# Performance work log

Measured on AMD Instinct MI355X. Metric: run time of the kernel, lower is better.

The kernel has to match this reference:

```python
import jax, jax.numpy as jnp
import numpy as np

EPS = 1e-8


def setup_inputs() -> dict:
    key = jax.random.key(0)
    kx, kw, kb = jax.random.split(key, 3)
    B, S, K, N = 64, 4096, 256, 256
    x = jax.random.normal(kx, (B, S, K), dtype=jnp.float32)
    # Kaiming-uniform-ish init for weight (out_features, in_features)
    bound_w = np.sqrt(6.0 / K) / np.sqrt(1.0 + 5.0)  # kaiming_uniform with a=sqrt(5)
    weight = jax.random.uniform(kw, (N, K), dtype=jnp.float32, minval=-bound_w, maxval=bound_w)
    bound_b = 1.0 / np.sqrt(K)
    bias = jax.random.uniform(kb, (N,), dtype=jnp.float32, minval=-bound_b, maxval=bound_b)
    return {"x": x, "weight": weight, "bias": bias}


def reference(x, weight, bias):
    """LNS inference path of LNSLinear.

    log_out[m, n] = logsumexp_k(log(|x[m,k]|+eps) + log(|w[n,k]|+eps))
    out = sign(sign(x) @ sign(w).T) * exp(log_out) + bias
    Computed stably as log(exp(lx - mx) @ exp(lw - mw).T) + mx + mw.
    """
    orig_shape = x.shape
    K = weight.shape[1]
    xf = x.reshape(-1, K)                                  # [M, K]
    log_x = jnp.log(jnp.abs(xf) + EPS)                     # [M, K]
    x_sign = jnp.sign(xf)                                  # [M, K]
    log_w = jnp.log(jnp.abs(weight) + EPS)                 # [N, K]
    w_sign = jnp.sign(weight)                              # [N, K]

    mx = jnp.max(log_x, axis=-1, keepdims=True)            # [M, 1]
    mw = jnp.max(log_w, axis=-1, keepdims=True)            # [N, 1]
    # logsumexp over k without materializing [M, N, K]
    acc = jnp.einsum('mk,nk->mn', jnp.exp(log_x - mx), jnp.exp(log_w - mw))
    log_out = jnp.log(acc) + mx + mw.T                     # [M, N]

    out_sign = jnp.sign(jnp.einsum('mk,nk->mn', x_sign, w_sign))
    out = out_sign * jnp.exp(log_out) + bias
    return out.reshape(orig_shape[:-1] + (weight.shape[0],))
```

## Files before the change

kernel.cpp:

```cpp
#include <hip/hip_runtime.h>
#include <hip/hip_bf16.h>
#include <stdint.h>


#define K_DIM 256
#define N_DIM 256
#define BM 128
#define BN 128
#define BK 32
#define LDK 40

typedef float f32x4 __attribute__((ext_vector_type(4)));
typedef __bf16 bf16x4 __attribute__((ext_vector_type(4)));
typedef __bf16 bf16x8 __attribute__((ext_vector_type(8)));
typedef unsigned short u16x4v __attribute__((ext_vector_type(4)));
typedef unsigned short u16x8v __attribute__((ext_vector_type(8)));

__device__ __forceinline__ void store_abs_sgn(float4 v, unsigned short* pa, unsigned short* ps) {
    bf16x4 h;
    h[0] = (__bf16)__builtin_fabsf(v.x);
    h[1] = (__bf16)__builtin_fabsf(v.y);
    h[2] = (__bf16)__builtin_fabsf(v.z);
    h[3] = (__bf16)__builtin_fabsf(v.w);
    unsigned int u0 = __float_as_uint(v.x), u1 = __float_as_uint(v.y);
    unsigned int u2 = __float_as_uint(v.z), u3 = __float_as_uint(v.w);
    u16x4v s;
    s[0] = (unsigned short)(0x3F80u | ((u0 >> 16) & 0x8000u));
    s[1] = (unsigned short)(0x3F80u | ((u1 >> 16) & 0x8000u));
    s[2] = (unsigned short)(0x3F80u | ((u2 >> 16) & 0x8000u));
    s[3] = (unsigned short)(0x3F80u | ((u3 >> 16) & 0x8000u));
    *(u16x4v*)pa = __builtin_bit_cast(u16x4v, h);
    *(u16x4v*)ps = s;
}

__global__ __launch_bounds__(256, 2)
void lns_gemm_kernel(const float* __restrict__ X, const float* __restrict__ W,
                     const float* __restrict__ bias, float* __restrict__ out, int M) {
    __shared__ unsigned short sAabs[BM * LDK];
    __shared__ unsigned short sAsgn[BM * LDK];
    __shared__ unsigned short sBabs[BN * LDK];
    __shared__ unsigned short sBsgn[BN * LDK];

    const int tid  = threadIdx.x;
    const int lane = tid & 63;
    const int wave = tid >> 6;
    const int quad = lane >> 4;
    const int l16  = lane & 15;
    const int mb   = blockIdx.y;
    const int nb   = blockIdx.x;
    const int wm   = (wave >> 1) * 64;
    const int wn   = (wave & 1) * 64;

    const float* Ax = X + (size_t)(mb * BM) * K_DIM;
    const float* Bw = W + (size_t)(nb * BN) * K_DIM;

    f32x4 accP[4][4];
    f32x4 accS[4][4];
#pragma unroll
    for (int i = 0; i < 4; ++i)
#pragma unroll
        for (int j = 0; j < 4; ++j) {
            accP[i][j] = (f32x4)(0.0f);
            accS[i][j] = (f32x4)(0.0f);
        }

    for (int k0 = 0; k0 < K_DIM; k0 += BK) {
        __syncthreads();
#pragma unroll
        for (int i = 0; i < 4; ++i) {
            int f   = i * 256 + tid;
            int row = f >> 3;
            int kc  = (f & 7) << 2;
            float4 va = *(const float4*)(Ax + (size_t)row * K_DIM + k0 + kc);
            store_abs_sgn(va, &sAabs[row * LDK + kc], &sAsgn[row * LDK + kc]);
            float4 vb = *(const float4*)(Bw + (size_t)row * K_DIM + k0 + kc);
            store_abs_sgn(vb, &sBabs[row * LDK + kc], &sBsgn[row * LDK + kc]);
        }
        __syncthreads();

        bf16x8 aab[4], asg[4], bab[4], bsg[4];
#pragma unroll
        for (int mi = 0; mi < 4; ++mi) {
            int off = (wm + mi * 16 + l16) * LDK + quad * 8;
            aab[mi] = __builtin_bit_cast(bf16x8, *(const u16x8v*)(sAabs + off));
            asg[mi] = __builtin_bit_cast(bf16x8, *(const u16x8v*)(sAsgn + off));
        }
#pragma unroll
        for (int ni = 0; ni < 4; ++ni) {
            int off = (wn + ni * 16 + l16) * LDK + quad * 8;
            bab[ni] = __builtin_bit_cast(bf16x8, *(const u16x8v*)(sBabs + off));
            bsg[ni] = __builtin_bit_cast(bf16x8, *(const u16x8v*)(sBsgn + off));
        }
#pragma unroll
        for (int mi = 0; mi < 4; ++mi)
#pragma unroll
            for (int ni = 0; ni < 4; ++ni) {
                accP[mi][ni] = __builtin_amdgcn_mfma_f32_16x16x32_bf16(
                    aab[mi], bab[ni], accP[mi][ni], 0, 0, 0);
                accS[mi][ni] = __builtin_amdgcn_mfma_f32_16x16x32_bf16(
                    asg[mi], bsg[ni], accS[mi][ni], 0, 0, 0);
            }
    }

#pragma unroll
    for (int ni = 0; ni < 4; ++ni) {
        int n   = nb * BN + wn + ni * 16 + l16;
        float b = bias[n];
#pragma unroll
        for (int mi = 0; mi < 4; ++mi) {
            int mbase = mb * BM + wm + mi * 16 + quad * 4;
#pragma unroll
            for (int r = 0; r < 4; ++r) {
                float p = accP[mi][ni][r];
                float s = accS[mi][ni][r];
                float v = (s > 0.0f) ? p : ((s < 0.0f) ? -p : 0.0f);
                out[(size_t)(mbase + r) * N_DIM + n] = v + b;
            }
        }
    }
}

extern "C" void kernel_launch(void* const* d_in, const int* in_sizes, int n_in,
                              void* d_out, int out_size, void* d_ws, size_t ws_size,
                              hipStream_t stream) {
    const float* x    = (const float*)d_in[0];
    const float* w    = (const float*)d_in[1];
    const float* bias = (const float*)d_in[2];
    float* out        = (float*)d_out;

    const int M = in_sizes[0] / K_DIM;

    dim3 grid(N_DIM / BN, M / BM, 1);
    dim3 block(256, 1, 1);
    lns_gemm_kernel<<<grid, block, 0, stream>>>(x, w, bias, out, M);
}
```

Measured before the change: 504.6 us.

## Double-buffer direct global-to-LDS loads and pre-convert weights to bf16 abs/sign

Adds a small pre-kernel that converts the weight matrix once per call into a packed bf16 abs/sign layout in the workspace. The main GEMM now copies raw fp32 X tiles and packed W tiles straight into swizzled LDS with global_load_lds and double buffering, overlapping the next tile's load with the current MFMAs. The abs/sign conversion of X moves to the LDS-read stage. This is meant to hide global memory latency and cut per-tile conversion and register traffic, at the cost of an extra kernel launch and more LDS per block.

After: 494.3 us. 2.0% less time.

```diff
diff --git a/kernel.cpp b/kernel.cpp
--- a/kernel.cpp
+++ b/kernel.cpp
@@ -8,38 +8,44 @@
 #define BM 128
 #define BN 128
 #define BK 32
-#define LDK 40
+#define NKBLK 8
 
 typedef float f32x4 __attribute__((ext_vector_type(4)));
-typedef __bf16 bf16x4 __attribute__((ext_vector_type(4)));
 typedef __bf16 bf16x8 __attribute__((ext_vector_type(8)));
 typedef unsigned short u16x4v __attribute__((ext_vector_type(4)));
 typedef unsigned short u16x8v __attribute__((ext_vector_type(8)));
 
-__device__ __forceinline__ void store_abs_sgn(float4 v, unsigned short* pa, unsigned short* ps) {
-    bf16x4 h;
-    h[0] = (__bf16)__builtin_fabsf(v.x);
-    h[1] = (__bf16)__builtin_fabsf(v.y);
-    h[2] = (__bf16)__builtin_fabsf(v.z);
-    h[3] = (__bf16)__builtin_fabsf(v.w);
-    unsigned int u0 = __float_as_uint(v.x), u1 = __float_as_uint(v.y);
-    unsigned int u2 = __float_as_uint(v.z), u3 = __float_as_uint(v.w);
-    u16x4v s;
-    s[0] = (unsigned short)(0x3F80u | ((u0 >> 16) & 0x8000u));
-    s[1] = (unsigned short)(0x3F80u | ((u1 >> 16) & 0x8000u));
-    s[2] = (unsigned short)(0x3F80u | ((u2 >> 16) & 0x8000u));
-    s[3] = (unsigned short)(0x3F80u | ((u3 >> 16) & 0x8000u));
-    *(u16x4v*)pa = __builtin_bit_cast(u16x4v, h);
-    *(u16x4v*)ps = s;
+__global__ void w_convert_kernel(const float* __restrict__ W, unsigned short* __restrict__ Wp) {
+    int t = blockIdx.x * 256 + threadIdx.x;
+    int n = t >> 6;
+    int k = (t & 63) << 2;
+    float4 v = *(const float4*)(W + (size_t)n * K_DIM + k);
+    unsigned short* row = Wp + ((size_t)n * NKBLK + (k >> 5)) * 64;
+    int pos = k & 31;
+    float vv[4] = {v.x, v.y, v.z, v.w};
+    u16x4v a, s;
+#pragma unroll
+    for (int j = 0; j < 4; ++j) {
+        __bf16 h = (__bf16)__builtin_fabsf(vv[j]);
+        a[j] = __builtin_bit_cast(unsigned short, h);
+        unsigned int u = __float_as_uint(vv[j]);
+        s[j] = (unsigned short)(0x3F80u | ((u >> 16) & 0x8000u));
+    }
+    *(u16x4v*)(row + pos) = a;
+    *(u16x4v*)(row + 32 + pos) = s;
+}
+
+__device__ __forceinline__ void gload_lds16(const void* g, void* l) {
+    __builtin_amdgcn_global_load_lds(
+        (const __attribute__((address_space(1))) unsigned int*)g,
+        (__attribute__((address_space(3))) unsigned int*)l, 16, 0, 0);
 }
 
 __global__ __launch_bounds__(256, 2)
-void lns_gemm_kernel(const float* __restrict__ X, const float* __restrict__ W,
-                     const float* __restrict__ bias, float* __restrict__ out, int M) {
-    __shared__ unsigned short sAabs[BM * LDK];
-    __shared__ unsigned short sAsgn[BM * LDK];
-    __shared__ unsigned short sBabs[BN * LDK];
-    __shared__ unsigned short sBsgn[BN * LDK];
+void lns_gemm_kernel(const float* __restrict__ X, const unsigned short* __restrict__ Wp,
+                     const float* __restrict__ bias, float* __restrict__ out) {
+    __shared__ __attribute__((aligned(16))) float sA[2][BM * BK];
+    __shared__ __attribute__((aligned(16))) unsigned short sB[2][BN * 64];
 
     const int tid  = threadIdx.x;
     const int lane = tid & 63;
@@ -52,7 +58,18 @@
     const int wn   = (wave & 1) * 64;
 
     const float* Ax = X + (size_t)(mb * BM) * K_DIM;
-    const float* Bw = W + (size_t)(nb * BN) * K_DIM;
+    const unsigned short* Bw = Wp + (size_t)(nb * BN) * (NKBLK * 64);
+
+    const float* gA[4];
+    const unsigned short* gB[4];
+#pragma unroll
+    for (int i = 0; i < 4; ++i) {
+        int f = i * 256 + tid;
+        int r = f >> 3;
+        int g = (f & 7) ^ (r & 7);
+        gA[i] = Ax + (size_t)r * K_DIM + g * 4;
+        gB[i] = Bw + ((size_t)r * NKBLK) * 64 + g * 8;
+    }
 
     f32x4 accP[4][4];
     f32x4 accS[4][4];
@@ -64,32 +81,66 @@
             accS[i][j] = (f32x4)(0.0f);
         }
 
-    for (int k0 = 0; k0 < K_DIM; k0 += BK) {
-        __syncthreads();
 #pragma unroll
-        for (int i = 0; i < 4; ++i) {
-            int f   = i * 256 + tid;
-            int row = f >> 3;
-            int kc  = (f & 7) << 2;
-            float4 va = *(const float4*)(Ax + (size_t)row * K_DIM + k0 + kc);
-            store_abs_sgn(va, &sAabs[row * LDK + kc], &sAsgn[row * LDK + kc]);
-            float4 vb = *(const float4*)(Bw + (size_t)row * K_DIM + k0 + kc);
-            store_abs_sgn(vb, &sBabs[row * LDK + kc], &sBsgn[row * LDK + kc]);
+    for (int i = 0; i < 4; ++i) {
+        gload_lds16(gA[i], &sA[0][(i * 256 + wave * 64) * 4]);
+        gA[i] += BK;
+    }
+#pragma unroll
+    for (int i = 0; i < 4; ++i) {
+        gload_lds16(gB[i], &sB[0][(i * 256 + wave * 64) * 8]);
+        gB[i] += 64;
+    }
+
+    for (int kb = 0; kb < NKBLK; ++kb) {
+        const int cur = kb & 1;
+        if (kb + 1 < NKBLK) {
+            const int nxt = cur ^ 1;
+#pragma unroll
+            for (int i = 0; i < 4; ++i) {
+                gload_lds16(gA[i], &sA[nxt][(i * 256 + wave * 64) * 4]);
+                gA[i] += BK;
+            }
+#pragma unroll
+            for (int i = 0; i < 4; ++i) {
+                gload_lds16(gB[i], &sB[nxt][(i * 256 + wave * 64) * 8]);
+                gB[i] += 64;
+            }
+            asm volatile("s_waitcnt vmcnt(8)\n\ts_barrier" ::: "memory");
+        } else {
+            asm volatile("s_waitcnt vmcnt(0)\n\ts_barrier" ::: "memory");
         }
-        __syncthreads();
 
         bf16x8 aab[4], asg[4], bab[4], bsg[4];
 #pragma unroll
         for (int mi = 0; mi < 4; ++mi) {
-            int off = (wm + mi * 16 + l16) * LDK + quad * 8;
-            aab[mi] = __builtin_bit_cast(bf16x8, *(const u16x8v*)(sAabs + off));
-            asg[mi] = __builtin_bit_cast(bf16x8, *(const u16x8v*)(sAsgn + off));
+            int m = wm + mi * 16 + l16;
+            const float* rowp = &sA[cur][m * BK];
+            int s0 = (2 * quad) ^ (m & 7);
+            f32x4 f0 = *(const f32x4*)(rowp + s0 * 4);
+            f32x4 f1 = *(const f32x4*)(rowp + (s0 ^ 1) * 4);
+            u16x8v ab, sg;
+#pragma unroll
+            for (int j = 0; j < 4; ++j) {
+                __bf16 h0 = (__bf16)__builtin_fabsf(f0[j]);
+                __bf16 h1 = (__bf16)__builtin_fabsf(f1[j]);
+                ab[j]     = __builtin_bit_cast(unsigned short, h0);
+                ab[j + 4] = __builtin_bit_cast(unsigned short, h1);
+                unsigned int u0 = __float_as_uint(f0[j]);
+                unsigned int u1 = __float_as_uint(f1[j]);
+                sg[j]     = (unsigned short)(0x3F80u | ((u0 >> 16) & 0x8000u));
+                sg[j + 4] = (unsigned short)(0x3F80u | ((u1 >> 16) & 0x8000u));
+            }
+            aab[mi] = __builtin_bit_cast(bf16x8, ab);
+            asg[mi] = __builtin_bit_cast(bf16x8, sg);
         }
 #pragma unroll
         for (int ni = 0; ni < 4; ++ni) {
-            int off = (wn + ni * 16 + l16) * LDK + quad * 8;
-            bab[ni] = __builtin_bit_cast(bf16x8, *(const u16x8v*)(sBabs + off));
-            bsg[ni] = __builtin_bit_cast(bf16x8, *(const u16x8v*)(sBsgn + off));
+            int r = wn + ni * 16 + l16;
+            const unsigned short* rp = &sB[cur][r * 64];
+            int sa = quad ^ (r & 7);
+            bab[ni] = __builtin_bit_cast(bf16x8, *(const u16x8v*)(rp + sa * 8));
+            bsg[ni] = __builtin_bit_cast(bf16x8, *(const u16x8v*)(rp + (sa ^ 4) * 8));
         }
 #pragma unroll
         for (int mi = 0; mi < 4; ++mi)
@@ -100,6 +151,8 @@
                 accS[mi][ni] = __builtin_amdgcn_mfma_f32_16x16x32_bf16(
                     asg[mi], bsg[ni], accS[mi][ni], 0, 0, 0);
             }
+
+        asm volatile("s_waitcnt lgkmcnt(0)\n\ts_barrier" ::: "memory");
     }
 
 #pragma unroll
@@ -127,10 +180,13 @@
     const float* w    = (const float*)d_in[1];
     const float* bias = (const float*)d_in[2];
     float* out        = (float*)d_out;
+    unsigned short* Wp = (unsigned short*)d_ws;
 
     const int M = in_sizes[0] / K_DIM;
 
+    w_convert_kernel<<<dim3(64, 1, 1), dim3(256, 1, 1), 0, stream>>>(w, Wp);
+
     dim3 grid(N_DIM / BN, M / BM, 1);
     dim3 block(256, 1, 1);
-    lns_gemm_kernel<<<grid, block, 0, stream>>>(x, w, bias, out, M);
+    lns_gemm_kernel<<<grid, block, 0, stream>>>(x, Wp, bias, out);
 }
```
